# Performance work log

Hardware: AMD Instinct MI355X
Metric: run time of the kernel (lower is better)

The kernel has to match this reference:

```python
import jax, jax.numpy as jnp
import numpy as np
import math

B, S, E, H = 2, 2048, 1024, 16
D = E // H  # d_head = 64

def setup_inputs() -> dict:
    key = jax.random.key(0)
    ks = jax.random.split(key, 7)
    query = jax.random.normal(ks[0], (B, S, E), dtype=jnp.float32)
    k_in = jax.random.normal(ks[1], (B, S, E), dtype=jnp.float32)
    v_in = jax.random.normal(ks[2], (B, S, E), dtype=jnp.float32)
    # causal mask, broadcastable over batch and heads; mask==0 positions are blocked
    mask = jnp.tril(jnp.ones((S, S), dtype=jnp.int32))[None, None]
    scale = 1.0 / math.sqrt(E)
    w_q = jax.random.normal(ks[3], (E, E), dtype=jnp.float32) * scale
    w_k = jax.random.normal(ks[4], (E, E), dtype=jnp.float32) * scale
    w_v = jax.random.normal(ks[5], (E, E), dtype=jnp.float32) * scale
    w_o = jax.random.normal(ks[6], (E, E), dtype=jnp.float32) * scale
    return {"query": query, "key": k_in, "value": v_in, "mask": mask,
            "w_q": w_q, "w_k": w_k, "w_v": w_v, "w_o": w_o}

def reference(query, key, value, mask, w_q, w_k, w_v, w_o):
    # projections (nn.Linear with no bias: x @ W^T); split heads -> [B,H,S,D]
    q = (query @ w_q.T).reshape(B, S, H, D).transpose(0, 2, 1, 3)
    k = (key @ w_k.T).reshape(B, S, H, D).transpose(0, 2, 1, 3)
    v = (value @ w_v.T).reshape(B, S, H, D).transpose(0, 2, 1, 3)
    # scaled dot-product scores [B,H,S,S]
    scores = jnp.einsum('bhqd,bhkd->bhqk', q, k) / math.sqrt(D)
    scores = jnp.where(mask == 0, jnp.float32(-1e9), scores)
    attn = jax.nn.softmax(scores, axis=-1)  # dropout p=0.0 -> identity
    out = jnp.einsum('bhqk,bhkd->bhqd', attn, v)  # [B,H,S,D]
    out = out.transpose(0, 2, 1, 3).reshape(B, S, E)
    return out @ w_o.T
```

## Files before the change

kernel.cpp:

```cpp
#include <hip/hip_runtime.h>
#include <hip/hip_bf16.h>

#define B_ 2
#define S_ 2048
#define E_ 1024
#define H_ 16
#define D_ 64

typedef __attribute__((ext_vector_type(8))) short bf16x8;
typedef __attribute__((ext_vector_type(4))) float f32x4;

static __device__ __forceinline__ unsigned short f2bf(float x) {
    union { float f; unsigned u; } v; v.f = x;
    unsigned r = v.u + 0x7FFF + ((v.u >> 16) & 1);
    return (unsigned short)(r >> 16);
}

static __device__ __forceinline__ unsigned pack2bf(float a, float b) {
    union { float f; unsigned u; } x, y; x.f = a; y.f = b;
    unsigned ra = x.u + 0x7FFF + ((x.u >> 16) & 1);
    unsigned rb = y.u + 0x7FFF + ((y.u >> 16) & 1);
    return (ra >> 16) | (rb & 0xFFFF0000u);
}

static __device__ __forceinline__ unsigned packtrunc(float a, float b) {
    union { float f; unsigned u; } x, y; x.f = a; y.f = b;
    return __builtin_amdgcn_perm(y.u, x.u, 0x07060302);
}

static __device__ __forceinline__ void async_copy16(const void* gsrc, void* ldst) {
    __builtin_amdgcn_global_load_lds(
        (const __attribute__((address_space(1))) void*)gsrc,
        (__attribute__((address_space(3))) void*)ldst, 16, 0, 0);
}

__global__ void cvt_all(const float* __restrict__ s0, const float* __restrict__ s1,
                        const float* __restrict__ s2, const float* __restrict__ s3,
                        const float* __restrict__ s4, const float* __restrict__ s5,
                        const float* __restrict__ s6,
                        unsigned short* __restrict__ xdst, unsigned short* __restrict__ wdst,
                        float scq) {
    int b = blockIdx.x;
    const float* src; unsigned short* dst; int i; float c = 1.f;
    if (b < 12288) {
        int ti = b >> 12, lb = b & 4095;
        src = (ti == 0) ? s0 : (ti == 1) ? s1 : s2;
        dst = xdst + (size_t)ti * 4194304;
        i = lb * 256 + threadIdx.x;
    } else {
        int r = b - 12288, ti = r >> 10, lb = r & 1023;
        src = (ti == 0) ? s3 : (ti == 1) ? s4 : (ti == 2) ? s5 : s6;
        dst = wdst + (size_t)ti * 1048576;
        i = lb * 256 + threadIdx.x;
        if (ti == 0) c = scq;
    }
    float4 f = ((const float4*)src)[i];
    ushort4 o;
    o.x = f2bf(f.x * c); o.y = f2bf(f.y * c); o.z = f2bf(f.z * c); o.w = f2bf(f.w * c);
    ((ushort4*)dst)[i] = o;
}

template <int MODE>
__global__ __launch_bounds__(256) void gemm128(
    const unsigned short* __restrict__ A0, const unsigned short* __restrict__ B0,
    void* __restrict__ C0, int M, int N, int K) {
    __shared__ __align__(16) unsigned short Al[2][128 * 64];
    __shared__ __align__(16) unsigned short Bl[2][128 * 64];
    const unsigned short* A = A0;
    const unsigned short* Bm = B0;
    int z = 0;
    if (MODE == 4) {
        z = blockIdx.z;
        A  = A0 + (size_t)z * 4194304;
        Bm = B0 + (size_t)z * 1048576;
    }
    const int o = (int)(blockIdx.x + (blockIdx.y << 3));
    const int cx = o & 7, tx = o >> 3;
    const int bm = ((cx << 2) + (tx >> 3)) * 128;
    const int bn = (tx & 7) * 128;
    const int tid = threadIdx.x;
    const int w = tid >> 6, lane = tid & 63;
    const int col = lane & 15, quad = lane >> 4, swz = col & 7;
    const int wm = (w >> 1) * 64, wn = (w & 1) * 64;

    f32x4 acc[4][4] = {};

#pragma unroll
    for (int it = 0; it < 4; it++) {
        int s = tid + it * 256, r = s >> 3, cg = (s & 7) ^ (r & 7);
        async_copy16(A + (size_t)(bm + r) * K + cg * 8, &Al[0][s * 8]);
        async_copy16(Bm + (size_t)(bn + r) * K + cg * 8, &Bl[0][s * 8]);
    }

    const int nk = K >> 6;
    for (int kt = 0; kt < nk; kt++) {
        const int cur = kt & 1;
        __syncthreads();
        if (kt + 1 < nk) {
            const int k1 = (kt + 1) << 6, nb = cur ^ 1;
#pragma unroll
            for (int it = 0; it < 4; it++) {
                int s = tid + it * 256, r = s >> 3, cg = (s & 7) ^ (r & 7);
                async_copy16(A + (size_t)(bm + r) * K + k1 + cg * 8, &Al[nb][s * 8]);
                async_copy16(Bm + (size_t)(bn + r) * K + k1 + cg * 8, &Bl[nb][s * 8]);
            }
        }
        const unsigned short* Ab = &Al[cur][0];
        const unsigned short* Bb = &Bl[cur][0];
#pragma unroll
        for (int h = 0; h < 2; h++) {
            const int cq = ((h * 4 + quad) ^ swz) * 8;
            bf16x8 af[4], bf[4];
#pragma unroll
            for (int i = 0; i < 4; i++) af[i] = *(const bf16x8*)&Ab[(wm + i * 16 + col) * 64 + cq];
#pragma unroll
            for (int j = 0; j < 4; j++) bf[j] = *(const bf16x8*)&Bb[(wn + j * 16 + col) * 64 + cq];
#pragma unroll
            for (int i = 0; i < 4; i++)
#pragma unroll
                for (int j = 0; j < 4; j++)
                    acc[i][j] = __builtin_amdgcn_mfma_f32_16x16x32_bf16(af[i], bf[j], acc[i][j], 0, 0, 0);
        }
    }

    if (MODE == 3) {
#pragma unroll
        for (int i = 0; i < 4; i++)
#pragma unroll
            for (int j = 0; j < 4; j++)
#pragma unroll
                for (int r = 0; r < 4; r++) {
                    int gm = bm + wm + i * 16 + quad * 4 + r;
                    int gn = bn + wn + j * 16 + col;
                    ((float*)C0)[(size_t)gm * N + gn] = acc[i][j][r];
                }
    } else {
        __syncthreads();
        unsigned short* scr = ((w < 2) ? &Al[0][0] : &Bl[0][0]) + (w & 1) * 4096;
        const int b  = (bm + wm) >> 11;
        const int s0 = (bm + wm) & 2047;
        const int hh = (bn + wn) >> 6;
        unsigned short* outp = (unsigned short*)C0 + (size_t)z * 4194304;
        if (z == 2) {
#pragma unroll
            for (int i = 0; i < 4; i++)
#pragma unroll
                for (int j = 0; j < 4; j++) {
                    int n = j * 16 + col;
                    int c = i * 2 + (quad >> 1);
                    uint2 pk;
                    pk.x = pack2bf(acc[i][j][0], acc[i][j][1]);
                    pk.y = pack2bf(acc[i][j][2], acc[i][j][3]);
                    *(uint2*)&scr[n * 64 + ((c ^ (n & 7)) << 3) + ((quad & 1) << 2)] = pk;
                }
#pragma unroll
            for (int it = 0; it < 8; it++) {
                int slot = it * 64 + lane, n = slot >> 3, c = slot & 7;
                uint4 v = *(uint4*)&scr[n * 64 + ((c ^ (n & 7)) << 3)];
                *(uint4*)&outp[(((size_t)b * H_ + hh) * D_ + n) * S_ + s0 + c * 8] = v;
            }
        } else {
#pragma unroll
            for (int i = 0; i < 4; i++)
#pragma unroll
                for (int j = 0; j < 4; j++)
#pragma unroll
                    for (int r = 0; r < 4; r++) {
                        int m = i * 16 + quad * 4 + r, n = j * 16 + col;
                        scr[m * 64 + (((n >> 3) ^ (m & 7)) << 3) + (n & 7)] = f2bf(acc[i][j][r]);
                    }
#pragma unroll
            for (int it = 0; it < 8; it++) {
                int slot = it * 64 + lane, m = slot >> 3, c = slot & 7;
                uint4 v = *(uint4*)&scr[m * 64 + ((c ^ (m & 7)) << 3)];
                *(uint4*)&outp[(((size_t)b * H_ + hh) * S_ + s0 + m) * (size_t)D_ + c * 8] = v;
            }
        }
    }
}

__global__ __launch_bounds__(512) void attn_kernel(
    const unsigned short* __restrict__ Q, const unsigned short* __restrict__ K_,
    const unsigned short* __restrict__ Vt, unsigned short* __restrict__ Out) {
    __shared__ __align__(16) unsigned short KV[8][4096];
    __shared__ __align__(16) float Lred[4][2][64];
    const int o = (int)(blockIdx.x + (blockIdx.y << 4));
    const int cx = o & 7, tx = o >> 3;
    const int hloc = (tx >> 1) & 3;
    const int f_ = (tx ^ (tx >> 5)) & 1;
    const int G_ = (((tx >> 4) & 1) << 2) | (((tx >> 3) & 1) << 1) | (tx & 1);
    const int qb = f_ ? (G_ ^ 15) : G_;
    const int bh = (cx << 2) + hloc;
    const int q0 = qb * 128;
    const int tid = threadIdx.x;
    const int w = tid >> 6, lane = tid & 63;
    const int qg = w >> 1, kh = w & 1, kh32 = kh << 5;
    const int col = lane & 15, quad = lane >> 4, swz = col & 7;
    const int qw0 = q0 + qg * 32;
    const float NINF = -__builtin_huge_valf();

    const unsigned short* Qh = Q + (size_t)bh * S_ * D_;
    const unsigned short* Kh = K_ + (size_t)bh * S_ * D_;
    const unsigned short* Vh = Vt + (size_t)bh * D_ * S_;

    bf16x8 qf[2][2];
#pragma unroll
    for (int i = 0; i < 2; i++)
#pragma unroll
        for (int h = 0; h < 2; h++)
            qf[i][h] = *(const bf16x8*)(Qh + (size_t)(qw0 + i * 16 + col) * 64 + h * 32 + quad * 8);

    f32x4 o_[2][4] = {};
    float lsum[2] = {0.f, 0.f};

    const int sRow = tid >> 3, sCg = (tid & 7) ^ (sRow & 7);
    const size_t koff = (size_t)sRow * 64 + sCg * 8;
    const size_t voff = (size_t)sRow * S_ + sCg * 8;
    const int ldsoff = tid * 8;

    const int nk = 2 * (qb + 1);

    async_copy16(Kh + koff, &KV[0][ldsoff]);
    async_copy16(Vh + voff, &KV[4][ldsoff]);
    async_copy16(Kh + koff + 64 * 64, &KV[1][ldsoff]);
    async_copy16(Vh + voff + 64, &KV[5][ldsoff]);

    for (int kt = 0; kt < nk; kt++) {
        const int k0 = kt * 64;
        {
            const int kp = kt + 2;
            const int src = (kp < nk) ? kp : (nk - 1);
            const int bp = kp & 3;
            async_copy16(Kh + koff + (size_t)src * 4096, &KV[bp][ldsoff]);
            async_copy16(Vh + voff + (size_t)src * 64, &KV[4 + bp][ldsoff]);
        }
        asm volatile("s_waitcnt vmcnt(4)" ::: "memory");
        __builtin_amdgcn_s_barrier();

        if (k0 + kh32 > qw0 + 31) continue;

        const unsigned short* Kb = &KV[kt & 3][0];
        const unsigned short* Vb = &KV[4 + (kt & 3)][0];

        f32x4 sc[2][2] = {};
#pragma unroll
        for (int h = 0; h < 2; h++) {
            const int cq = ((h * 4 + quad) ^ swz) * 8;
#pragma unroll
            for (int ct = 0; ct < 2; ct++) {
                bf16x8 kf = *(const bf16x8*)&Kb[(kh32 + ct * 16 + col) * 64 + cq];
                sc[0][ct] = __builtin_amdgcn_mfma_f32_16x16x32_bf16(kf, qf[0][h], sc[0][ct], 0, 0, 0);
                sc[1][ct] = __builtin_amdgcn_mfma_f32_16x16x32_bf16(kf, qf[1][h], sc[1][ct], 0, 0, 0);
            }
        }
        if (k0 + kh32 + 31 <= qw0) {
#pragma unroll
            for (int i = 0; i < 2; i++)
#pragma unroll
                for (int ct = 0; ct < 2; ct++) {
#pragma unroll
                    for (int r = 0; r < 4; r++)
                        sc[i][ct][r] = __builtin_amdgcn_exp2f(sc[i][ct][r]);
                    lsum[i] += (sc[i][ct][0] + sc[i][ct][1]) + (sc[i][ct][2] + sc[i][ct][3]);
                }
        } else {
#pragma unroll
            for (int i = 0; i < 2; i++)
#pragma unroll
                for (int ct = 0; ct < 2; ct++) {
#pragma unroll
                    for (int r = 0; r < 4; r++) {
                        int key = k0 + kh32 + ct * 16 + quad * 4 + r;
                        int qidx = qw0 + i * 16 + col;
                        float s = (key <= qidx) ? sc[i][ct][r] : NINF;
                        sc[i][ct][r] = __builtin_amdgcn_exp2f(s);
                    }
                    lsum[i] += (sc[i][ct][0] + sc[i][ct][1]) + (sc[i][ct][2] + sc[i][ct][3]);
                }
        }
        union { bf16x8 v; unsigned u[4]; } pf[2];
#pragma unroll
        for (int i = 0; i < 2; i++) {
            pf[i].u[0] = packtrunc(sc[i][0][0], sc[i][0][1]);
            pf[i].u[1] = packtrunc(sc[i][0][2], sc[i][0][3]);
            pf[i].u[2] = packtrunc(sc[i][1][0], sc[i][1][1]);
            pf[i].u[3] = packtrunc(sc[i][1][2], sc[i][1][3]);
        }
#pragma unroll
        for (int dt = 0; dt < 4; dt++) {
            const int row = dt * 16 + col;
            const int ko0 = kh32 + quad * 4;
            const int ko1 = ko0 + 16;
            union { bf16x8 v; uint2 d2[2]; } vf;
            vf.d2[0] = *(const uint2*)&Vb[row * 64 + (((ko0 >> 3) ^ (row & 7)) << 3) + (ko0 & 7)];
            vf.d2[1] = *(const uint2*)&Vb[row * 64 + (((ko1 >> 3) ^ (row & 7)) << 3) + (ko1 & 7)];
#pragma unroll
            for (int i = 0; i < 2; i++)
                o_[i][dt] = __builtin_amdgcn_mfma_f32_16x16x32_bf16(vf.v, pf[i].v, o_[i][dt], 0, 0, 0);
        }
    }

    __syncthreads();
    if (kh == 1) {
        f32x4* R = (f32x4*)&KV[0][0] + qg * 512 + lane * 8;
#pragma unroll
        for (int i = 0; i < 2; i++)
#pragma unroll
            for (int dt = 0; dt < 4; dt++) R[i * 4 + dt] = o_[i][dt];
        Lred[qg][0][lane] = lsum[0];
        Lred[qg][1][lane] = lsum[1];
    }
    __syncthreads();
    if (kh == 0) {
        f32x4* R = (f32x4*)&KV[0][0] + qg * 512 + lane * 8;
#pragma unroll
        for (int i = 0; i < 2; i++)
#pragma unroll
            for (int dt = 0; dt < 4; dt++) o_[i][dt] += R[i * 4 + dt];
        lsum[0] += Lred[qg][0][lane];
        lsum[1] += Lred[qg][1][lane];

        const int b = bh >> 4, hh = bh & 15;
#pragma unroll
        for (int i = 0; i < 2; i++) {
            float l = lsum[i];
            l += __shfl_xor(l, 16);
            l += __shfl_xor(l, 32);
            float inv = 1.f / l;
            int gq = qw0 + i * 16 + col;
#pragma unroll
            for (int dt = 0; dt < 4; dt++) {
                uint2 pk;
                pk.x = pack2bf(o_[i][dt][0] * inv, o_[i][dt][1] * inv);
                pk.y = pack2bf(o_[i][dt][2] * inv, o_[i][dt][3] * inv);
                *(uint2*)&Out[((size_t)b * S_ + gq) * E_ + hh * 64 + dt * 16 + quad * 4] = pk;
            }
        }
    }
}

extern "C" void kernel_launch(void* const* d_in, const int* in_sizes, int n_in,
                              void* d_out, int out_size, void* d_ws, size_t ws_size,
                              hipStream_t stream) {
    const float* query = (const float*)d_in[0];
    const float* key_i = (const float*)d_in[1];
    const float* value = (const float*)d_in[2];
    const float* w_q = (const float*)d_in[4];
    const float* w_k = (const float*)d_in[5];
    const float* w_v = (const float*)d_in[6];
    const float* w_o = (const float*)d_in[7];
    float* out = (float*)d_out;

    const int M = B_ * S_;
    const int N = E_, K = E_;

    char* ws = (char*)d_ws;
    unsigned short* xq  = (unsigned short*)(ws);
    unsigned short* wqb = (unsigned short*)(ws + (24u << 20));
    unsigned short* Qb  = (unsigned short*)(ws + (32u << 20));
    unsigned short* Kb  = (unsigned short*)(ws + (40u << 20));
    unsigned short* Vtb = (unsigned short*)(ws + (48u << 20));
    unsigned short* Ab  = (unsigned short*)(ws + (56u << 20));

    const float SCQ = 0.125f * 1.44269504088896f;

    cvt_all<<<16384, 256, 0, stream>>>(query, key_i, value, w_q, w_k, w_v, w_o,
                                       xq, wqb, SCQ);

    gemm128<4><<<dim3(N / 128, M / 128, 3), 256, 0, stream>>>(xq, wqb, Qb, M, N, K);

    attn_kernel<<<dim3(S_ / 128, B_ * H_), 512, 0, stream>>>(Qb, Kb, Vtb, Ab);

    gemm128<3><<<dim3(N / 128, M / 128), 256, 0, stream>>>(
        Ab, wqb + 3u * 1048576u, out, M, N, K);
}
```

Baseline: 211.7 us.

## Use 4-stage K=32 LDS pipeline in GEMM and raise wave priority around attention MFMAs

The projection GEMM moves from a double-buffered K=64 tile loop with a full __syncthreads per step to a 4-slot ring of K=32 tiles. Loads are issued two steps ahead and synchronised with s_waitcnt vmcnt plus a bare s_barrier, with a new XOR swizzle for the 32-wide rows. The goal is more latency hiding for global-to-LDS copies, at the cost of twice as many loop iterations and barriers. The attention kernel also wraps its MFMA blocks in s_setprio(1)/s_setprio(0) so the scheduler favours waves issuing matrix ops.

```diff
diff --git a/kernel.cpp b/kernel.cpp
--- a/kernel.cpp
+++ b/kernel.cpp
@@ -64,8 +64,7 @@
 __global__ __launch_bounds__(256) void gemm128(
     const unsigned short* __restrict__ A0, const unsigned short* __restrict__ B0,
     void* __restrict__ C0, int M, int N, int K) {
-    __shared__ __align__(16) unsigned short Al[2][128 * 64];
-    __shared__ __align__(16) unsigned short Bl[2][128 * 64];
+    __shared__ __align__(16) unsigned short KV[8][4096];
     const unsigned short* A = A0;
     const unsigned short* Bm = B0;
     int z = 0;
@@ -80,48 +79,60 @@
     const int bn = (tx & 7) * 128;
     const int tid = threadIdx.x;
     const int w = tid >> 6, lane = tid & 63;
-    const int col = lane & 15, quad = lane >> 4, swz = col & 7;
+    const int col = lane & 15, quad = lane >> 4;
     const int wm = (w >> 1) * 64, wn = (w & 1) * 64;
+    const int cq = (quad ^ ((col >> 1) & 3)) << 3;
 
     f32x4 acc[4][4] = {};
 
-#pragma unroll
-    for (int it = 0; it < 4; it++) {
-        int s = tid + it * 256, r = s >> 3, cg = (s & 7) ^ (r & 7);
-        async_copy16(A + (size_t)(bm + r) * K + cg * 8, &Al[0][s * 8]);
-        async_copy16(Bm + (size_t)(bn + r) * K + cg * 8, &Bl[0][s * 8]);
-    }
-
-    const int nk = K >> 6;
+    const int r0 = tid >> 2;
+    const int cg = (tid & 3) ^ ((r0 >> 1) & 3);
+    const size_t aoff0 = (size_t)(bm + r0) * K + cg * 8;
+    const size_t aoff1 = (size_t)(bm + r0 + 64) * K + cg * 8;
+    const size_t boff0 = (size_t)(bn + r0) * K + cg * 8;
+    const size_t boff1 = (size_t)(bn + r0 + 64) * K + cg * 8;
+    const int l0 = tid * 8, l1 = (tid + 256) * 8;
+
+    const int nk = K >> 5;
+
+    async_copy16(A  + aoff0,      &KV[0][l0]);
+    async_copy16(A  + aoff1,      &KV[0][l1]);
+    async_copy16(Bm + boff0,      &KV[4][l0]);
+    async_copy16(Bm + boff1,      &KV[4][l1]);
+    async_copy16(A  + aoff0 + 32, &KV[1][l0]);
+    async_copy16(A  + aoff1 + 32, &KV[1][l1]);
+    async_copy16(Bm + boff0 + 32, &KV[5][l0]);
+    async_copy16(Bm + boff1 + 32, &KV[5][l1]);
+
     for (int kt = 0; kt < nk; kt++) {
-        const int cur = kt & 1;
-        __syncthreads();
-        if (kt + 1 < nk) {
-            const int k1 = (kt + 1) << 6, nb = cur ^ 1;
-#pragma unroll
-            for (int it = 0; it < 4; it++) {
-                int s = tid + it * 256, r = s >> 3, cg = (s & 7) ^ (r & 7);
-                async_copy16(A + (size_t)(bm + r) * K + k1 + cg * 8, &Al[nb][s * 8]);
-                async_copy16(Bm + (size_t)(bn + r) * K + k1 + cg * 8, &Bl[nb][s * 8]);
-            }
-        }
-        const unsigned short* Ab = &Al[cur][0];
-        const unsigned short* Bb = &Bl[cur][0];
-#pragma unroll
-        for (int h = 0; h < 2; h++) {
-            const int cq = ((h * 4 + quad) ^ swz) * 8;
-            bf16x8 af[4], bf[4];
-#pragma unroll
-            for (int i = 0; i < 4; i++) af[i] = *(const bf16x8*)&Ab[(wm + i * 16 + col) * 64 + cq];
-#pragma unroll
-            for (int j = 0; j < 4; j++) bf[j] = *(const bf16x8*)&Bb[(wn + j * 16 + col) * 64 + cq];
-#pragma unroll
-            for (int i = 0; i < 4; i++)
-#pragma unroll
-                for (int j = 0; j < 4; j++)
-                    acc[i][j] = __builtin_amdgcn_mfma_f32_16x16x32_bf16(af[i], bf[j], acc[i][j], 0, 0, 0);
-        }
-    }
+        {
+            const int kp = kt + 2;
+            const int src = (kp < nk) ? kp : (nk - 1);
+            const int bp = kp & 3;
+            const size_t ko = (size_t)src * 32;
+            async_copy16(A  + aoff0 + ko, &KV[bp][l0]);
+            async_copy16(A  + aoff1 + ko, &KV[bp][l1]);
+            async_copy16(Bm + boff0 + ko, &KV[4 + bp][l0]);
+            async_copy16(Bm + boff1 + ko, &KV[4 + bp][l1]);
+        }
+        asm volatile("s_waitcnt vmcnt(8)" ::: "memory");
+        __builtin_amdgcn_s_barrier();
+
+        const unsigned short* Ab = &KV[kt & 3][0];
+        const unsigned short* Bb = &KV[4 + (kt & 3)][0];
+        bf16x8 af[4], bfr[4];
+#pragma unroll
+        for (int i = 0; i < 4; i++) af[i]  = *(const bf16x8*)&Ab[(wm + i * 16 + col) * 32 + cq];
+#pragma unroll
+        for (int j = 0; j < 4; j++) bfr[j] = *(const bf16x8*)&Bb[(wn + j * 16 + col) * 32 + cq];
+#pragma unroll
+        for (int i = 0; i < 4; i++)
+#pragma unroll
+            for (int j = 0; j < 4; j++)
+                acc[i][j] = __builtin_amdgcn_mfma_f32_16x16x32_bf16(af[i], bfr[j], acc[i][j], 0, 0, 0);
+    }
+
+    __syncthreads();
 
     if (MODE == 3) {
 #pragma unroll
@@ -135,8 +146,7 @@
                     ((float*)C0)[(size_t)gm * N + gn] = acc[i][j][r];
                 }
     } else {
-        __syncthreads();
-        unsigned short* scr = ((w < 2) ? &Al[0][0] : &Bl[0][0]) + (w & 1) * 4096;
+        unsigned short* scr = &KV[w * 2][0];
         const int b  = (bm + wm) >> 11;
         const int s0 = (bm + wm) & 2047;
         const int hh = (bn + wn) >> 6;
@@ -243,6 +253,7 @@
         const unsigned short* Vb = &KV[4 + (kt & 3)][0];
 
         f32x4 sc[2][2] = {};
+        __builtin_amdgcn_s_setprio(1);
 #pragma unroll
         for (int h = 0; h < 2; h++) {
             const int cq = ((h * 4 + quad) ^ swz) * 8;
@@ -253,6 +264,7 @@
                 sc[1][ct] = __builtin_amdgcn_mfma_f32_16x16x32_bf16(kf, qf[1][h], sc[1][ct], 0, 0, 0);
             }
         }
+        __builtin_amdgcn_s_setprio(0);
         if (k0 + kh32 + 31 <= qw0) {
 #pragma unroll
             for (int i = 0; i < 2; i++)
@@ -286,6 +298,7 @@
             pf[i].u[2] = packtrunc(sc[i][1][0], sc[i][1][1]);
             pf[i].u[3] = packtrunc(sc[i][1][2], sc[i][1][3]);
         }
+        __builtin_amdgcn_s_setprio(1);
 #pragma unroll
         for (int dt = 0; dt < 4; dt++) {
             const int row = dt * 16 + col;
@@ -298,6 +311,7 @@
             for (int i = 0; i < 2; i++)
                 o_[i][dt] = __builtin_amdgcn_mfma_f32_16x16x32_bf16(vf.v, pf[i].v, o_[i][dt], 0, 0, 0);
         }
+        __builtin_amdgcn_s_setprio(0);
     }
 
     __syncthreads();
```

Result: no change. 207.9 us (-1.8%).
